# Kernel tuning notes

Hardware: AMD Instinct MI355X
Metric: run time of the kernel (lower is better)

The kernel has to match this reference:

```python
import jax, jax.numpy as jnp
import numpy as np

FS = 16            # fixStride
LAST_RATIO = 0.5
TAUA, TAUB = 10.0, 0.1
TOT_EPOCHS = 100
EPS = 1e-20
SEED = 777


def _safe_norm(diff):
    # ||diff||_2 with subgradient 0 at 0 (matches torch.norm backward at 0)
    sq = jnp.sum(diff * diff, axis=-1)
    d = jnp.sqrt(jnp.where(sq > 0, sq, 1.0))
    return jnp.where(sq > 0, d, 0.0)


def _forward(x, w_score, b_score, att_params, num_graphs, epoch):
    BN, C = x.shape
    B = int(num_graphs)
    N = BN // B
    RES = N - FS + 1                       # rows per graph (unfold1d)
    MAXP = int(np.ceil(N * LAST_RATIO))    # max_pivot_count = ceil(N*last_ratio/init_ratio)

    # --- TopKPool scorer (init_ratio==1.0): permute nodes per graph by desc score
    scores = (x @ w_score + b_score) / jnp.sqrt(jnp.sum(w_score ** 2))
    perm = jnp.argsort(-scores.reshape(B, N), axis=-1, stable=True)      # [B,N]
    xg = jnp.take_along_axis(x.reshape(B, N, C), perm[..., None], axis=1)

    # --- sliding-window edges: row r -> dests r..r+FS-1, src node r
    dst = jnp.arange(RES)[:, None] + jnp.arange(FS)[None, :]             # [RES,FS]
    x_src = xg[:, :RES, :]                                               # [B,RES,C]
    x_dst = xg[:, dst, :]                                                # [B,RES,FS,C]

    # getSM_ei + scatter_softmax over rows: att = [x_s, x_d] @ att_params
    a1, a2 = att_params[:C], att_params[C:]
    sm = jax.nn.softmax((xg @ a1)[:, :RES, None] + (xg @ a2)[:, dst], axis=-1)  # [B,RES,FS]

    # getDM_ei (sigma=1): gaussian-kernel edge distances
    gk = jnp.exp(-_safe_norm(x_src[:, :, None, :] - x_dst) / 2.0) - EPS  # [B,RES,FS]

    # scatterSort: stable descending sort of gk per row
    order = jnp.argsort(-gk, axis=-1, stable=True)
    gk_sort = jnp.take_along_axis(gk, order, axis=-1)
    sm_sort = jnp.take_along_axis(sm, order, axis=-1)

    # per-rank column logits: scatter-sum of sorted attention over rows of each graph
    logits = jnp.broadcast_to(sm_sort.sum(axis=1)[:, None, :], (B, RES, FS))
    logits = logits.at[:, :, 0].set(-jnp.inf)            # mask rank-0 (self edge)

    # gumbel-softmax with annealed temperature
    tau0 = TAUA * (TAUB / TAUA) ** (float(epoch) / TOT_EPOCHS)
    g = jax.random.gumbel(jax.random.key(SEED), (B, RES, FS), jnp.float32)
    gmb = jax.nn.softmax((g + logits) / tau0, axis=-1)

    # per-row threshold and shifted distances (unsorted layout)
    ths = jnp.sum(gk_sort * gmb, axis=-1, keepdims=True)
    shifted = jax.nn.relu(gk - ths)                      # [B,RES,FS]

    # scatter_min over positions 1..FS-1 (position 0 excluded via index redirect)
    delta = (jnp.argmin(shifted[:, :, 1:], axis=-1) + 1).astype(jnp.int32)  # [B,RES]

    # innerLoopStar: follow skip pointers from row 0, up to MAXP pivots
    def chain(delta_g):
        def step(ptr, _):
            valid = ptr < RES
            piv = jnp.where(valid, ptr, -1)
            nxt = jnp.where(valid, ptr + delta_g[jnp.clip(ptr, 0, RES - 1)], jnp.int32(RES))
            return nxt, piv
        _, pivs = jax.lax.scan(step, jnp.int32(0), None, length=MAXP)
        return pivs

    pivots = jax.vmap(chain)(delta)                      # [B,MAXP], -1 padded
    mask = pivots >= 0
    pooled = jnp.take_along_axis(xg, jnp.clip(pivots, 0, N - 1)[..., None], axis=1)
    pooled = pooled * mask[..., None]                    # [B,MAXP,C]
    return pooled, shifted, pivots


def setup_inputs() -> dict:
    key = jax.random.key(0)
    k0, k1, k2, k3 = jax.random.split(key, 4)
    B, N, C = 128, 512, 64
    return {
        "x": jax.random.normal(k0, (B * N, C), jnp.float32),
        "w_score": jax.random.normal(k1, (C,), jnp.float32),
        "b_score": jax.random.normal(k2, (), jnp.float32),
        "att_params": jax.random.normal(k3, (2 * C,), jnp.float32),
        "num_graphs": B,
        "epoch": 10,
    }


def reference(x, w_score, b_score, att_params, num_graphs, epoch):
    return _forward(x, w_score, b_score, att_params, num_graphs, epoch)
```

## Files before the change

kernel.cpp:

```cpp
#include <hip/hip_runtime.h>
#include <math.h>

#define BB 128
#define NN 512
#define CC 64
#define FS 16
#define RES 497
#define MAXP 256
#define BN (BB*NN)
#define GT (BB*RES*FS)
#define WPB 16
#define NCH 32
#define ROWS (WPB+FS-1)
#define PITCH 66
#define GW2 256

__device__ __forceinline__ unsigned rotl32(unsigned x, int d){ return (x<<d)|(x>>(32-d)); }

__device__ __forceinline__ void threefry777(unsigned x0, unsigned x1, unsigned &o0, unsigned &o1){
  const unsigned ks0 = 0u, ks1 = 777u;
  const unsigned ks2 = 0x1BD11BDAu ^ ks0 ^ ks1;
  x0 += ks0; x1 += ks1;
  x0+=x1; x1=rotl32(x1,13); x1^=x0;
  x0+=x1; x1=rotl32(x1,15); x1^=x0;
  x0+=x1; x1=rotl32(x1,26); x1^=x0;
  x0+=x1; x1=rotl32(x1, 6); x1^=x0;
  x0+=ks1; x1+=ks2+1u;
  x0+=x1; x1=rotl32(x1,17); x1^=x0;
  x0+=x1; x1=rotl32(x1,29); x1^=x0;
  x0+=x1; x1=rotl32(x1,16); x1^=x0;
  x0+=x1; x1=rotl32(x1,24); x1^=x0;
  x0+=ks2; x1+=ks0+2u;
  x0+=x1; x1=rotl32(x1,13); x1^=x0;
  x0+=x1; x1=rotl32(x1,15); x1^=x0;
  x0+=x1; x1=rotl32(x1,26); x1^=x0;
  x0+=x1; x1=rotl32(x1, 6); x1^=x0;
  x0+=ks0; x1+=ks1+3u;
  x0+=x1; x1=rotl32(x1,17); x1^=x0;
  x0+=x1; x1=rotl32(x1,29); x1^=x0;
  x0+=x1; x1=rotl32(x1,16); x1^=x0;
  x0+=x1; x1=rotl32(x1,24); x1^=x0;
  x0+=ks1; x1+=ks2+4u;
  x0+=x1; x1=rotl32(x1,13); x1^=x0;
  x0+=x1; x1=rotl32(x1,15); x1^=x0;
  x0+=x1; x1=rotl32(x1,26); x1^=x0;
  x0+=x1; x1=rotl32(x1, 6); x1^=x0;
  x0+=ks2; x1+=ks0+5u;
  o0 = x0; o1 = x1;
}

__device__ __forceinline__ float gumbel_at_f32(unsigned p){
  unsigned o0, o1;
  threefry777(0u, p, o0, o1);
  unsigned bits = o0 ^ o1;
  float fl = __uint_as_float((bits >> 9) | 0x3f800000u) - 1.0f;
  float u  = fmaxf(1.17549435e-38f, fl);
  return -logf(-logf(u));
}

__device__ __forceinline__ double wave_push_f64(double v, int dstLane){
  int lo = __double2loint(v), hi = __double2hiint(v);
  int plo = __builtin_amdgcn_ds_permute(dstLane<<2, lo);
  int phi = __builtin_amdgcn_ds_permute(dstLane<<2, hi);
  return __hiloint2double(phi, plo);
}

__global__ __launch_bounds__(NN) void k_scoresort(const float* __restrict__ x,
    const float* __restrict__ w, const float* __restrict__ bsc,
    const float* __restrict__ att, double* __restrict__ s1s,
    double* __restrict__ s2s, int* __restrict__ perm){
  int b = blockIdx.x, t = threadIdx.x;
  __shared__ double ss[NN];
  __shared__ int    si[NN];
  __shared__ double l1[NN], l2[NN];

  double wn=0.0, dw=0.0, d1=0.0, d2=0.0;
  #pragma unroll
  for (int c=0;c<CC;c++){ double wv=(double)w[c]; wn += wv*wv; }
  const float4* xr = (const float4*)(x + (size_t)(b*NN+t)*CC);
  #pragma unroll
  for (int q=0;q<CC/4;q++){
    float4 v = xr[q];
    double xv;
    xv=(double)v.x; dw+=xv*(double)w[4*q+0]; d1+=xv*(double)att[4*q+0]; d2+=xv*(double)att[CC+4*q+0];
    xv=(double)v.y; dw+=xv*(double)w[4*q+1]; d1+=xv*(double)att[4*q+1]; d2+=xv*(double)att[CC+4*q+1];
    xv=(double)v.z; dw+=xv*(double)w[4*q+2]; d1+=xv*(double)att[4*q+2]; d2+=xv*(double)att[CC+4*q+2];
    xv=(double)v.w; dw+=xv*(double)w[4*q+3]; d1+=xv*(double)att[4*q+3]; d2+=xv*(double)att[CC+4*q+3];
  }
  double s = (dw + (double)bsc[0]) / sqrt(wn);
  int idx = t;
  l1[t] = d1;
  l2[t] = d2;

  for (int k = 2; k <= NN; k <<= 1){
    bool up = ((t & k) == 0);
    for (int j = k >> 1; j >= 64; j >>= 1){
      ss[t] = s; si[t] = idx;
      __syncthreads();
      double os = ss[t ^ j]; int oi = si[t ^ j];
      bool first = ((t & j) == 0);
      bool cmp = (s > os) || (s == os && idx < oi);
      bool keep = (cmp == (first == up));
      if (!keep){ s = os; idx = oi; }
      __syncthreads();
    }
    #pragma unroll
    for (int j = 32; j > 0; j >>= 1){
      if (j <= (k >> 1)){
        double os = __shfl_xor(s, j, 64);
        int    oi = __shfl_xor(idx, j, 64);
        bool first = ((t & j) == 0);
        bool cmp = (s > os) || (s == os && idx < oi);
        bool keep = (cmp == (first == up));
        if (!keep){ s = os; idx = oi; }
      }
    }
  }
  __syncthreads();
  perm[b*NN + t] = idx;
  s1s[b*NN + t] = l1[idx];
  s2s[b*NN + t] = l2[idx];
}

__global__ __launch_bounds__(256) void k_passA(const float* __restrict__ x,
    const int* __restrict__ perm, const double* __restrict__ s1s,
    const double* __restrict__ s2s, double* __restrict__ gkd,
    unsigned char* __restrict__ rank8, double* __restrict__ partial){
  int b = blockIdx.y, ch = blockIdx.x, tid = threadIdx.x;
  int i0 = ch*WPB;
  int nwin  = min(WPB, RES - i0);
  int nrows = min(ROWS, NN - i0);
  __shared__ float  xs[ROWS*PITCH];
  __shared__ int    pg[ROWS];
  __shared__ double wred[4][FS];

  if (tid < nrows) pg[tid] = perm[b*NN + i0 + tid];
  __syncthreads();
  for (int u = tid; u < nrows*16; u += 256){
    int r = u >> 4, seg = u & 15;
    float4 v = ((const float4*)(x + (size_t)(b*NN + pg[r])*CC))[seg];
    float2* dst = (float2*)&xs[r*PITCH + seg*4];
    dst[0] = make_float2(v.x, v.y);
    dst[1] = make_float2(v.z, v.w);
  }
  __syncthreads();

  int w = tid >> 4, j = tid & 15;
  int lane = tid & 63, gbase = lane & 48, wv = tid >> 6;
  bool act = (w < nwin);
  int i = i0 + w;

  double sq = 0.0;
  const float* rs = &xs[w*PITCH];
  const float* rd = &xs[(w+j)*PITCH];
  #pragma unroll
  for (int c2=0;c2<CC/2;c2++){
    float2 a  = *(const float2*)&rs[2*c2];
    float2 bb = *(const float2*)&rd[2*c2];
    double d0 = (double)a.x - (double)bb.x;
    double d1v= (double)a.y - (double)bb.y;
    sq += d0*d0;
    sq += d1v*d1v;
  }
  double d   = (sq > 0.0) ? sqrt(sq) : 0.0;
  double gkv = exp(-d*0.5) - 1e-20;

  int drow = min(i + j, NN-1);
  double smt = s1s[b*NN + i] + s2s[b*NN + drow];
  double m = smt;
  #pragma unroll
  for (int off=8; off; off>>=1) m = fmax(m, __shfl_xor(m, off, 16));
  double em = exp(smt - m);
  double ssum = em;
  #pragma unroll
  for (int off=8; off; off>>=1) ssum += __shfl_xor(ssum, off, 16);
  double smn = em / ssum;

  int rank = 0;
  #pragma unroll
  for (int k=0;k<16;k++){
    double gkk = __shfl(gkv, gbase + k, 64);
    rank += ((gkk > gkv) || (gkk == gkv && k < j)) ? 1 : 0;
  }

  if (act){
    size_t base = ((size_t)b*RES + i)*FS;
    gkd[base + j]   = gkv;
    rank8[base + j] = (unsigned char)rank;
  }

  double contrib = act ? smn : 0.0;
  double srt = wave_push_f64(contrib, gbase + rank);
  srt += __shfl_xor(srt, 16, 64);
  srt += __shfl_xor(srt, 32, 64);
  if (lane < FS) wred[wv][lane] = srt;
  __syncthreads();
  if (tid < FS){
    partial[((size_t)b*NCH + ch)*FS + tid] =
        wred[0][tid] + wred[1][tid] + wred[2][tid] + wred[3][tid];
  }
}

__global__ __launch_bounds__(256) void k_gumbel(const double* __restrict__ gkd,
    const unsigned char* __restrict__ rank8, const double* __restrict__ partial,
    const int* __restrict__ epoch_p, float* __restrict__ shifted_out,
    int* __restrict__ delta){
  int b = blockIdx.y, tid = threadIdx.x;
  int win = blockIdx.x*GW2 + tid;
  __shared__ double pl[NCH*FS];
  __shared__ double cs[FS];
  __shared__ double glds[256*17];

  for (int u = tid; u < NCH*FS; u += 256) pl[u] = partial[(size_t)b*NCH*FS + u];
  __syncthreads();
  if (tid < FS){
    double a = 0.0;
    #pragma unroll
    for (int ch=0; ch<NCH; ch++) a += pl[ch*FS + tid];
    cs[tid] = a;
  }
  __syncthreads();

  if (win >= RES) return;
  double tau = 10.0 * pow(0.01, (double)epoch_p[0] / 100.0);
  size_t base = ((size_t)b*RES + win)*FS;

  double gk[FS];
  #pragma unroll
  for (int j=0;j<FS;j++) gk[j] = gkd[base + j];

  double z[FS];
  z[0] = 0.0;
  #pragma unroll
  for (int s=1;s<FS;s++){
    double g = (double)gumbel_at_f32((unsigned)(base + (unsigned)s));
    z[s] = (g + cs[s]) / tau;
  }
  double m = z[1];
  #pragma unroll
  for (int s=2;s<FS;s++) m = fmax(m, z[s]);

  double e[FS]; double ssum = 0.0;
  e[0] = 0.0;
  #pragma unroll
  for (int s=1;s<FS;s++){ e[s] = exp(z[s] - m); ssum += e[s]; }

  int base17 = tid*17;
  #pragma unroll
  for (int j=0;j<FS;j++){
    int rk = (int)rank8[base + j];
    glds[base17 + rk] = gk[j];
  }
  double ths = 0.0;
  #pragma unroll
  for (int s=0;s<FS;s++){
    ths += glds[base17 + s] * (e[s] / ssum);
  }

  double bv = 0.0; int bj = 1;
  #pragma unroll
  for (int j=0;j<FS;j++){
    double shv = fmax(gk[j] - ths, 0.0);
    shifted_out[base + j] = (float)shv;
    if (j == 1){ bv = shv; bj = 1; }
    else if (j > 1 && shv < bv){ bv = shv; bj = j; }
  }
  delta[b*RES + win] = bj;
}

__global__ __launch_bounds__(256) void k_chainpool(const int* __restrict__ delta,
    const int* __restrict__ perm, const float* __restrict__ x,
    float* __restrict__ piv_out, float* __restrict__ pooled){
  int b = blockIdx.x, tid = threadIdx.x;
  __shared__ int tbl[8][512];
  __shared__ int pivS[MAXP];

  for (int i = tid; i < 512; i += 256){
    int v;
    if (i < RES){ v = i + delta[b*RES + i]; if (v > RES) v = RES; }
    else v = RES;
    tbl[0][i] = v;
  }
  __syncthreads();
  #pragma unroll
  for (int k=1;k<8;k++){
    int v0 = tbl[k-1][tid];
    int v1 = tbl[k-1][tid+256];
    tbl[k][tid]     = tbl[k-1][v0];
    tbl[k][tid+256] = tbl[k-1][v1];
    __syncthreads();
  }
  {
    int p = 0;
    #pragma unroll
    for (int k=0;k<8;k++) if ((tid>>k)&1) p = tbl[k][p];
    int piv = (p < RES) ? p : -1;
    pivS[tid] = piv;
    piv_out[b*MAXP + tid] = (float)piv;
  }
  __syncthreads();

  for (int u = tid; u < MAXP*16; u += 256){
    int bp = u >> 4, seg = u & 15;
    int piv = pivS[bp];
    float4 v = make_float4(0.f,0.f,0.f,0.f);
    if (piv >= 0){
      int src = perm[b*NN + piv];
      v = ((const float4*)(x + (size_t)(b*NN + src)*CC))[seg];
    }
    ((float4*)pooled)[(size_t)(b*MAXP + bp)*16 + seg] = v;
  }
}

extern "C" void kernel_launch(void* const* d_in, const int* in_sizes, int n_in,
                              void* d_out, int out_size, void* d_ws, size_t ws_size,
                              hipStream_t stream) {
  (void)in_sizes; (void)n_in; (void)out_size; (void)ws_size;
  const float* x    = (const float*)d_in[0];
  const float* w    = (const float*)d_in[1];
  const float* bsc  = (const float*)d_in[2];
  const float* att  = (const float*)d_in[3];
  const int*   epch = (const int*)d_in[5];

  double* s1s     = (double*)d_ws;
  double* s2s     = s1s + BN;
  double* gkd     = s2s + BN;
  double* partial = gkd + GT;
  int*    perm    = (int*)(partial + (size_t)BB*NCH*FS);
  int*    delta   = perm + BN;
  unsigned char* rank8 = (unsigned char*)(delta + BB*RES);

  float* out_pooled  = (float*)d_out;
  float* out_shifted = out_pooled + BB*MAXP*CC;
  float* out_piv     = out_shifted + (size_t)BB*RES*FS;

  k_scoresort<<<BB, NN, 0, stream>>>(x, w, bsc, att, s1s, s2s, perm);
  k_passA    <<<dim3(NCH, BB), 256, 0, stream>>>(x, perm, s1s, s2s, gkd, rank8, partial);
  k_gumbel   <<<dim3((RES + GW2 - 1)/GW2, BB), GW2, 0, stream>>>(gkd, rank8, partial, epch, out_shifted, delta);
  k_chainpool<<<BB, 256, 0, stream>>>(delta, perm, x, out_piv, out_pooled);
}
```

Measured before the change: 62.29 us.

## Restructure gumbel kernel with coalesced LDS staging and factored softmax exponentials

Rewrites the gumbel/threshold kernel to stage each block's gk rows and rank bytes into LDS through coalesced double2/uint4 loads instead of per-thread strided reads. The softmax is factored as exp(g/tau)*exp(cs/tau), with the per-column factor computed once per block, which removes the max pass. Shifted outputs are written as float4. Blocks shrink to 128 threads across 4 chunks for more parallelism. Dropping the max subtraction risks overflow if cs/tau is large, and exp(a/tau) may differ numerically from the reference.

```diff
diff --git a/kernel.cpp b/kernel.cpp
--- a/kernel.cpp
+++ b/kernel.cpp
@@ -13,7 +13,8 @@
 #define NCH 32
 #define ROWS (WPB+FS-1)
 #define PITCH 66
-#define GW2 256
+#define TWPB 128
+#define TCH 4
 
 __device__ __forceinline__ unsigned rotl32(unsigned x, int d){ return (x<<d)|(x>>(32-d)); }
 
@@ -201,69 +202,78 @@
   }
 }
 
-__global__ __launch_bounds__(256) void k_gumbel(const double* __restrict__ gkd,
+__global__ __launch_bounds__(TWPB) void k_tail(const double* __restrict__ gkd,
     const unsigned char* __restrict__ rank8, const double* __restrict__ partial,
     const int* __restrict__ epoch_p, float* __restrict__ shifted_out,
     int* __restrict__ delta){
   int b = blockIdx.y, tid = threadIdx.x;
-  int win = blockIdx.x*GW2 + tid;
+  int w0 = blockIdx.x*TWPB;
+  int nw = min(TWPB, RES - w0);
   __shared__ double pl[NCH*FS];
-  __shared__ double cs[FS];
-  __shared__ double glds[256*17];
-
-  for (int u = tid; u < NCH*FS; u += 256) pl[u] = partial[(size_t)b*NCH*FS + u];
+  __shared__ double Ks[FS];
+  __shared__ double gkL[TWPB*17];
+  __shared__ double eL[TWPB*17];
+  __shared__ uint4  rkL[TWPB];
+
+  for (int u = tid; u < NCH*FS; u += TWPB) pl[u] = partial[(size_t)b*NCH*FS + u];
+  {
+    const double2* gsrc = (const double2*)(gkd + ((size_t)b*RES + w0)*FS);
+    for (int u = tid; u < nw*8; u += TWPB){
+      double2 v = gsrc[u];
+      int row = u >> 3, col = (u & 7) << 1;
+      gkL[row*17 + col]     = v.x;
+      gkL[row*17 + col + 1] = v.y;
+    }
+  }
+  if (tid < nw) rkL[tid] = ((const uint4*)rank8)[(size_t)b*RES + w0 + tid];
   __syncthreads();
   if (tid < FS){
     double a = 0.0;
     #pragma unroll
     for (int ch=0; ch<NCH; ch++) a += pl[ch*FS + tid];
-    cs[tid] = a;
-  }
-  __syncthreads();
-
-  if (win >= RES) return;
-  double tau = 10.0 * pow(0.01, (double)epoch_p[0] / 100.0);
+    double tauB = 10.0 * exp(-4.605170185988091 * ((double)epoch_p[0] / 100.0));
+    Ks[tid] = (tid == 0) ? 0.0 : exp(a / tauB);
+  }
+  __syncthreads();
+
+  if (tid >= nw) return;
+  int win = w0 + tid;
   size_t base = ((size_t)b*RES + win)*FS;
-
-  double gk[FS];
-  #pragma unroll
-  for (int j=0;j<FS;j++) gk[j] = gkd[base + j];
-
-  double z[FS];
-  z[0] = 0.0;
-  #pragma unroll
+  double tau = 10.0 * exp(-4.605170185988091 * ((double)epoch_p[0] / 100.0));
+  int gb = tid*17;
+
+  eL[gb] = 0.0;
+  double ssum = 0.0;
   for (int s=1;s<FS;s++){
-    double g = (double)gumbel_at_f32((unsigned)(base + (unsigned)s));
-    z[s] = (g + cs[s]) / tau;
-  }
-  double m = z[1];
-  #pragma unroll
-  for (int s=2;s<FS;s++) m = fmax(m, z[s]);
-
-  double e[FS]; double ssum = 0.0;
-  e[0] = 0.0;
-  #pragma unroll
-  for (int s=1;s<FS;s++){ e[s] = exp(z[s] - m); ssum += e[s]; }
-
-  int base17 = tid*17;
+    float g = gumbel_at_f32((unsigned)(base + (unsigned)s));
+    double E = exp((double)g / tau) * Ks[s];
+    eL[gb + s] = E;
+    ssum += E;
+  }
+
+  uint4 rw = rkL[tid];
+  unsigned rr[4] = { rw.x, rw.y, rw.z, rw.w };
+  double ths = 0.0;
   #pragma unroll
   for (int j=0;j<FS;j++){
-    int rk = (int)rank8[base + j];
-    glds[base17 + rk] = gk[j];
-  }
-  double ths = 0.0;
-  #pragma unroll
-  for (int s=0;s<FS;s++){
-    ths += glds[base17 + s] * (e[s] / ssum);
+    int rk = (int)((rr[j>>2] >> ((j&3)*8)) & 15u);
+    ths += gkL[gb + j] * (eL[gb + rk] / ssum);
   }
 
   double bv = 0.0; int bj = 1;
   #pragma unroll
-  for (int j=0;j<FS;j++){
-    double shv = fmax(gk[j] - ths, 0.0);
-    shifted_out[base + j] = (float)shv;
-    if (j == 1){ bv = shv; bj = 1; }
-    else if (j > 1 && shv < bv){ bv = shv; bj = j; }
+  for (int q=0;q<4;q++){
+    float4 sv;
+    float* svp = (float*)&sv;
+    #pragma unroll
+    for (int r=0;r<4;r++){
+      int j = q*4 + r;
+      double shv = fmax(gkL[gb + j] - ths, 0.0);
+      svp[r] = (float)shv;
+      if (j == 1){ bv = shv; bj = 1; }
+      else if (j > 1 && shv < bv){ bv = shv; bj = j; }
+    }
+    ((float4*)(shifted_out + base))[q] = sv;
   }
   delta[b*RES + win] = bj;
 }
@@ -336,6 +346,6 @@
 
   k_scoresort<<<BB, NN, 0, stream>>>(x, w, bsc, att, s1s, s2s, perm);
   k_passA    <<<dim3(NCH, BB), 256, 0, stream>>>(x, perm, s1s, s2s, gkd, rank8, partial);
-  k_gumbel   <<<dim3((RES + GW2 - 1)/GW2, BB), GW2, 0, stream>>>(gkd, rank8, partial, epch, out_shifted, delta);
+  k_tail     <<<dim3(TCH, BB), TWPB, 0, stream>>>(gkd, rank8, partial, epch, out_shifted, delta);
   k_chainpool<<<BB, 256, 0, stream>>>(delta, perm, x, out_piv, out_pooled);
 }
```

New measurement: 70.18 us. 1.13x slower.
